# Kernel tuning notes

Hardware: AMD Instinct MI355X
Metric: run time of the kernel (lower is better)

## Reference

```python
import jax, jax.numpy as jnp
import numpy as np

HID = 2560
NH, P, N, G, K = 80, 64, 128, 1, 4
INTER = NH * P            # 5120
CONV_DIM = INTER + 2 * G * N  # 5376
PROJ = INTER + CONV_DIM + NH  # 10576
EPS = 1e-5
DT_MIN, DT_MAX = 0.0, 100.0
BATCH = 64


def setup_inputs() -> dict:
    key = jax.random.key(0)
    ks = jax.random.split(key, 11)
    return {
        "input_states": jax.random.normal(ks[0], (BATCH, 1, HID), jnp.float32),
        "conv_state": 0.1 * jax.random.normal(ks[1], (BATCH, CONV_DIM, K), jnp.float32),
        "ssm_state": 0.1 * jax.random.normal(ks[2], (BATCH, NH, P, N), jnp.float32),
        "in_proj_w": jax.random.normal(ks[3], (PROJ, HID), jnp.float32) * (HID ** -0.5),
        "conv_w": jax.random.normal(ks[4], (CONV_DIM, K), jnp.float32) * 0.2,
        "conv_b": jax.random.normal(ks[5], (CONV_DIM,), jnp.float32) * 0.02,
        "dt_bias": jax.random.normal(ks[6], (NH,), jnp.float32) * 0.1,
        "A_log": jnp.log(jnp.arange(1, NH + 1, dtype=jnp.float32)),
        "D": jnp.ones((NH,), jnp.float32),
        "norm_w": jnp.ones((INTER,), jnp.float32),
        "out_proj_w": jax.random.normal(ks[7], (HID, INTER), jnp.float32) * (INTER ** -0.5),
    }


def reference(input_states, conv_state, ssm_state, in_proj_w, conv_w, conv_b,
              dt_bias, A_log, D, norm_w, out_proj_w):
    B = input_states.shape[0]
    # in_proj: (B,1,HID) @ (HID,PROJ) -> (B,1,PROJ); d_mlp == 0 with these dims
    proj = jnp.einsum("bsh,ph->bsp", input_states, in_proj_w)
    gate = proj[..., :INTER]                       # (B,1,INTER)
    hBC = proj[..., INTER:INTER + CONV_DIM]        # (B,1,CONV_DIM)
    dt = proj[..., INTER + CONV_DIM:]              # (B,1,NH)

    # conv cache update: roll left, append current token
    new_conv_state = jnp.concatenate(
        [conv_state[:, :, 1:], hBC[:, 0, :, None]], axis=-1)  # (B,CONV_DIM,K)
    x = jnp.sum(new_conv_state * conv_w[None], axis=-1) + conv_b  # (B,CONV_DIM)
    x = jax.nn.silu(x)

    hs = x[:, :INTER].reshape(B, NH, P)            # (B,NH,P)
    Bm = x[:, INTER:INTER + G * N].reshape(B, G, N)
    Cm = x[:, INTER + G * N:].reshape(B, G, N)
    Bm = jnp.repeat(Bm, NH // G, axis=1)           # (B,NH,N)
    Cm = jnp.repeat(Cm, NH // G, axis=1)           # (B,NH,N)

    # discretization (dt is per-head, broadcast over head_dim as in source)
    dt_sp = jnp.clip(jax.nn.softplus(dt[:, 0, :] + dt_bias), DT_MIN, DT_MAX)  # (B,NH)
    A = -jnp.exp(A_log)                            # (NH,)
    dA = jnp.exp(dt_sp * A)                        # (B,NH)

    dBx = dt_sp[:, :, None, None] * Bm[:, :, None, :] * hs[..., None]  # (B,NH,P,N)
    new_ssm = ssm_state * dA[:, :, None, None] + dBx                   # (B,NH,P,N)

    y = jnp.einsum("bhpn,bhn->bhp", new_ssm, Cm)   # (B,NH,P)
    y = y + hs * D[None, :, None]
    y = y.reshape(B, 1, INTER)

    # gated RMSNorm (fp32 internals)
    yf = y.astype(jnp.float32) * jax.nn.silu(gate.astype(jnp.float32))
    var = jnp.mean(yf * yf, axis=-1, keepdims=True)
    yn = norm_w * (yf * jax.lax.rsqrt(var + EPS)).astype(y.dtype)

    out = jnp.einsum("bsi,hi->bsh", yn, out_proj_w)  # (B,1,HID)
    return out
```

## Files before the change

### kernel.cpp

```cpp
#include <hip/hip_runtime.h>
#include <stdint.h>

#define HID 2560
#define NH 80
#define PDIM 64
#define NDIM 128
#define INTER 5120
#define CONV_DIM 5376
#define PROJ_DIM 10576
#define NBATCH 64
#define EPS_ 1e-5f

typedef short short8 __attribute__((ext_vector_type(8)));
typedef float f32x4 __attribute__((ext_vector_type(4)));

__device__ __forceinline__ unsigned short f2bf(float f){
  unsigned u = __builtin_bit_cast(unsigned, f);
  u += 0x7FFFu + ((u >> 16) & 1u);
  return (unsigned short)(u >> 16);
}
__device__ __forceinline__ float silu_(float x){ return x / (1.f + __expf(-x)); }

__global__ __launch_bounds__(256) void k_dt(const float* __restrict__ X,
                                            const float* __restrict__ W,
                                            float* __restrict__ dt_part,
                                            unsigned short* __restrict__ Xb){
  const int h = blockIdx.x, ks = blockIdx.y;
  const int tid = threadIdx.x, wid = tid >> 6, lane = tid & 63;
  const float* wr = W + (size_t)(INTER + CONV_DIM + h) * HID + ks * 320;
  float w[5];
  #pragma unroll
  for (int i = 0; i < 5; ++i) w[i] = wr[lane + i * 64];
  #pragma unroll
  for (int bi = 0; bi < 16; ++bi){
    const int b = wid * 16 + bi;
    const float* xr = X + (size_t)b * HID + ks * 320;
    float x[5];
    float acc = 0.f;
    #pragma unroll
    for (int i = 0; i < 5; ++i){ x[i] = xr[lane + i * 64]; acc += x[i] * w[i]; }
    if (h == 0){
      #pragma unroll
      for (int i = 0; i < 5; ++i)
        Xb[(size_t)b * HID + ks * 320 + lane + i * 64] = f2bf(x[i]);
    }
    #pragma unroll
    for (int m = 32; m; m >>= 1) acc += __shfl_xor(acc, m);
    if (lane == 0) dt_part[(ks * NBATCH + b) * NH + h] = acc;
  }
}

__global__ __launch_bounds__(64) void k1_proj(const unsigned short* __restrict__ Xb,
                                              const float* __restrict__ W,
                                              float* __restrict__ proj){
  const int lane = threadIdx.x;
  const int lr = lane & 15, lg = lane >> 4;
  const int n0 = blockIdx.x * 16;
  const short* ap = (const short*)Xb + (size_t)lr * HID + lg * 8;
  const float* bp = W + (size_t)(n0 + lr) * HID + lg * 8;
  f32x4 acc0 = {0,0,0,0}, acc1 = {0,0,0,0}, acc2 = {0,0,0,0}, acc3 = {0,0,0,0};
  #pragma unroll 4
  for (int s = 0; s < 80; ++s){
    const int k = s * 32;
    short8 a0 = *(const short8*)(ap + k);
    short8 a1 = *(const short8*)(ap + 16 * HID + k);
    short8 a2 = *(const short8*)(ap + 32 * HID + k);
    short8 a3 = *(const short8*)(ap + 48 * HID + k);
    float4 b0 = *(const float4*)(bp + k);
    float4 b1 = *(const float4*)(bp + k + 4);
    short8 bb;
    bb[0] = (short)f2bf(b0.x); bb[1] = (short)f2bf(b0.y);
    bb[2] = (short)f2bf(b0.z); bb[3] = (short)f2bf(b0.w);
    bb[4] = (short)f2bf(b1.x); bb[5] = (short)f2bf(b1.y);
    bb[6] = (short)f2bf(b1.z); bb[7] = (short)f2bf(b1.w);
    acc0 = __builtin_amdgcn_mfma_f32_16x16x32_bf16(a0, bb, acc0, 0, 0, 0);
    acc1 = __builtin_amdgcn_mfma_f32_16x16x32_bf16(a1, bb, acc1, 0, 0, 0);
    acc2 = __builtin_amdgcn_mfma_f32_16x16x32_bf16(a2, bb, acc2, 0, 0, 0);
    acc3 = __builtin_amdgcn_mfma_f32_16x16x32_bf16(a3, bb, acc3, 0, 0, 0);
  }
  #pragma unroll
  for (int r = 0; r < 4; ++r){
    const int m = lg * 4 + r;
    proj[(size_t)(m     ) * PROJ_DIM + n0 + lr] = acc0[r];
    proj[(size_t)(m + 16) * PROJ_DIM + n0 + lr] = acc1[r];
    proj[(size_t)(m + 32) * PROJ_DIM + n0 + lr] = acc2[r];
    proj[(size_t)(m + 48) * PROJ_DIM + n0 + lr] = acc3[r];
  }
}

__global__ __launch_bounds__(256) void k2a(const float* __restrict__ cs,
                                           const float* __restrict__ cw,
                                           const float* __restrict__ cb,
                                           const float* __restrict__ proj,
                                           const float* __restrict__ dt_part,
                                           const float* __restrict__ dt_bias,
                                           const float* __restrict__ A_log,
                                           float* __restrict__ hs_bc,
                                           float* __restrict__ dt_sp,
                                           float* __restrict__ dAv,
                                           float* __restrict__ s_bc){
  const int b = blockIdx.y;
  const int c0 = blockIdx.x * 384;
  const int tid = threadIdx.x;
  __shared__ float bc[384];
  for (int i = tid; i < 384; i += 256){
    const int c = c0 + i;
    float4 s4 = *(const float4*)(cs + ((size_t)b * CONV_DIM + c) * 4);
    float4 w4 = *(const float4*)(cw + (size_t)c * 4);
    float hbc = proj[(size_t)b * PROJ_DIM + INTER + c];
    float x = s4.y * w4.x + s4.z * w4.y + s4.w * w4.z + hbc * w4.w + cb[c];
    float v = silu_(x);
    hs_bc[(size_t)b * CONV_DIM + c] = v;
    if (blockIdx.x == 13) bc[i] = v;
  }
  if (blockIdx.x == 0 && tid < NH){
    float acc = dt_bias[tid];
    #pragma unroll
    for (int ks = 0; ks < 8; ++ks) acc += dt_part[(ks * NBATCH + b) * NH + tid];
    float sp = acc > 15.f ? acc : log1pf(__expf(acc));
    sp = fminf(fmaxf(sp, 0.f), 100.f);
    dt_sp[b * NH + tid] = sp;
    dAv[b * NH + tid] = __expf(-sp * __expf(A_log[tid]));
  }
  if (blockIdx.x == 13){
    __syncthreads();
    if (tid < 64){
      float p = bc[128 + tid] * bc[256 + tid] + bc[192 + tid] * bc[320 + tid];
      #pragma unroll
      for (int m = 32; m; m >>= 1) p += __shfl_xor(p, m);
      if (tid == 0) s_bc[b] = p;
    }
  }
}

__global__ __launch_bounds__(256) void k2b(const float* __restrict__ ssm,
                                           const float* __restrict__ hs_bc,
                                           const float* __restrict__ proj,
                                           const float* __restrict__ dt_sp,
                                           const float* __restrict__ dAv,
                                           const float* __restrict__ s_bc,
                                           const float* __restrict__ Dp,
                                           const float* __restrict__ norm_w,
                                           unsigned short* __restrict__ yfb,
                                           float* __restrict__ ssq_part){
  const int h = blockIdx.x, b = blockIdx.y;
  const int tid = threadIdx.x;
  const int wid = tid >> 6, lane = tid & 63;
  const int lr = lane & 15, lg = lane >> 4;
  const float dA_s = dAv[b * NH + h];
  const float coef = dt_sp[b * NH + h] * s_bc[b] + Dp[h];
  const float* Cb = hs_bc + (size_t)b * CONV_DIM + INTER + NDIM;
  float4 c0 = *(const float4*)(Cb + lr * 8);
  float4 c1 = *(const float4*)(Cb + lr * 8 + 4);
  const float* srow = ssm + ((size_t)b * NH + h) * PDIM * NDIM;
  float ssq = 0.f;
  __shared__ float ssql[4];
  #pragma unroll
  for (int r = 0; r < 4; ++r){
    const int p = wid * 16 + r * 4 + lg;
    const float* sp_ = srow + (size_t)p * NDIM + lr * 8;
    float4 v0 = *(const float4*)(sp_);
    float4 v1 = *(const float4*)(sp_ + 4);
    float dot = v0.x*c0.x + v0.y*c0.y + v0.z*c0.z + v0.w*c0.w
              + v1.x*c1.x + v1.y*c1.y + v1.z*c1.z + v1.w*c1.w;
    dot += __shfl_xor(dot, 1); dot += __shfl_xor(dot, 2);
    dot += __shfl_xor(dot, 4); dot += __shfl_xor(dot, 8);
    if (lr == 0){
      const int hp = h * PDIM + p;
      float hs = hs_bc[(size_t)b * CONV_DIM + hp];
      float y = dA_s * dot + hs * coef;
      float g = proj[(size_t)b * PROJ_DIM + hp];
      float yf = y * silu_(g) * norm_w[hp];
      yfb[(size_t)b * INTER + hp] = f2bf(yf);
      ssq += yf * yf;
    }
  }
  #pragma unroll
  for (int m = 32; m; m >>= 1) ssq += __shfl_xor(ssq, m);
  if (lane == 0) ssql[wid] = ssq;
  __syncthreads();
  if (tid == 0) ssq_part[b * NH + h] = ssql[0] + ssql[1] + ssql[2] + ssql[3];
}

__global__ __launch_bounds__(64) void k3_out(const unsigned short* __restrict__ Yb,
                                             const float* __restrict__ W,
                                             float* __restrict__ part){
  const int lane = threadIdx.x;
  const int lr = lane & 15, lg = lane >> 4;
  const int n0 = blockIdx.x * 16;
  const int ks = blockIdx.y;
  const int kb = ks * 1280;
  const short* ap = (const short*)Yb + (size_t)lr * INTER + kb + lg * 8;
  const float* bp = W + (size_t)(n0 + lr) * INTER + kb + lg * 8;
  f32x4 acc0 = {0,0,0,0}, acc1 = {0,0,0,0}, acc2 = {0,0,0,0}, acc3 = {0,0,0,0};
  #pragma unroll 4
  for (int s = 0; s < 40; ++s){
    const int k = s * 32;
    short8 a0 = *(const short8*)(ap + k);
    short8 a1 = *(const short8*)(ap + 16 * INTER + k);
    short8 a2 = *(const short8*)(ap + 32 * INTER + k);
    short8 a3 = *(const short8*)(ap + 48 * INTER + k);
    float4 b0 = *(const float4*)(bp + k);
    float4 b1 = *(const float4*)(bp + k + 4);
    short8 bb;
    bb[0] = (short)f2bf(b0.x); bb[1] = (short)f2bf(b0.y);
    bb[2] = (short)f2bf(b0.z); bb[3] = (short)f2bf(b0.w);
    bb[4] = (short)f2bf(b1.x); bb[5] = (short)f2bf(b1.y);
    bb[6] = (short)f2bf(b1.z); bb[7] = (short)f2bf(b1.w);
    acc0 = __builtin_amdgcn_mfma_f32_16x16x32_bf16(a0, bb, acc0, 0, 0, 0);
    acc1 = __builtin_amdgcn_mfma_f32_16x16x32_bf16(a1, bb, acc1, 0, 0, 0);
    acc2 = __builtin_amdgcn_mfma_f32_16x16x32_bf16(a2, bb, acc2, 0, 0, 0);
    acc3 = __builtin_amdgcn_mfma_f32_16x16x32_bf16(a3, bb, acc3, 0, 0, 0);
  }
  float* pt = part + (size_t)ks * NBATCH * 2560;
  #pragma unroll
  for (int r = 0; r < 4; ++r){
    const int m = lg * 4 + r;
    pt[(size_t)(m     ) * 2560 + n0 + lr] = acc0[r];
    pt[(size_t)(m + 16) * 2560 + n0 + lr] = acc1[r];
    pt[(size_t)(m + 32) * 2560 + n0 + lr] = acc2[r];
    pt[(size_t)(m + 48) * 2560 + n0 + lr] = acc3[r];
  }
}

__global__ __launch_bounds__(256) void k4_norm(const float* __restrict__ part,
                                               const float* __restrict__ ssq_part,
                                               float* __restrict__ out){
  const int b = blockIdx.y;
  const int tid = threadIdx.x;
  __shared__ float w4[4];
  __shared__ float sc;
  float v = (tid < NH) ? ssq_part[b * NH + tid] : 0.f;
  #pragma unroll
  for (int m = 32; m; m >>= 1) v += __shfl_xor(v, m);
  const int wid = tid >> 6, lane = tid & 63;
  if (lane == 0) w4[wid] = v;
  __syncthreads();
  if (tid == 0){
    float total = w4[0] + w4[1] + w4[2] + w4[3];
    sc = rsqrtf(total / (float)INTER + EPS_);
  }
  __syncthreads();
  const int j = blockIdx.x * 256 + tid;
  const size_t idx = (size_t)b * 2560 + j;
  const size_t plane = (size_t)NBATCH * 2560;
  float s = part[idx] + part[plane + idx] + part[2*plane + idx] + part[3*plane + idx];
  out[idx] = sc * s;
}

extern "C" void kernel_launch(void* const* d_in, const int* in_sizes, int n_in,
                              void* d_out, int out_size, void* d_ws, size_t ws_size,
                              hipStream_t stream){
  const float* x_in       = (const float*)d_in[0];
  const float* conv_state = (const float*)d_in[1];
  const float* ssm_state  = (const float*)d_in[2];
  const float* in_proj_w  = (const float*)d_in[3];
  const float* conv_w     = (const float*)d_in[4];
  const float* conv_b     = (const float*)d_in[5];
  const float* dt_bias    = (const float*)d_in[6];
  const float* A_log      = (const float*)d_in[7];
  const float* Dp         = (const float*)d_in[8];
  const float* norm_w     = (const float*)d_in[9];
  const float* out_proj_w = (const float*)d_in[10];
  float* out = (float*)d_out;

  char* ws = (char*)d_ws;
  unsigned short* Xb   = (unsigned short*)(ws);
  float* dt_part       = (float*)(ws + 327680);
  float* proj          = (float*)(ws + 491520);
  float* hs_bc         = (float*)(ws + 3198976);
  float* dt_sp         = (float*)(ws + 4575232);
  float* dAv           = (float*)(ws + 4595712);
  float* s_bc          = (float*)(ws + 4616192);
  float* ssq           = (float*)(ws + 4616448);
  unsigned short* Yb   = (unsigned short*)(ws + 4636928);
  float* part          = (float*)(ws + 5292288);

  k_dt<<<dim3(NH, 8), dim3(256), 0, stream>>>(x_in, in_proj_w, dt_part, Xb);
  k1_proj<<<dim3(PROJ_DIM / 16), dim3(64), 0, stream>>>(Xb, in_proj_w, proj);
  k2a<<<dim3(14, NBATCH), dim3(256), 0, stream>>>(conv_state, conv_w, conv_b, proj,
                                                  dt_part, dt_bias, A_log,
                                                  hs_bc, dt_sp, dAv, s_bc);
  k2b<<<dim3(NH, NBATCH), dim3(256), 0, stream>>>(ssm_state, hs_bc, proj, dt_sp, dAv,
                                                  s_bc, Dp, norm_w, Yb, ssq);
  k3_out<<<dim3(160, 4), dim3(64), 0, stream>>>(Yb, out_proj_w, part);
  k4_norm<<<dim3(10, NBATCH), dim3(256), 0, stream>>>(part, ssq, out);
}
```

Before: 136.5 us.

## Split-K both projection GEMMs into sixteen slices and reduce partials in consumers

The input projection now runs as a split-K GEMM over 16 K-slices, each writing its own partial plane. The conv/gate consumers (k2a, k2b) sum those 16 planes when they read proj values. The output projection goes from 4 to 16 K-slices, and the final norm kernel sums 16 partial planes. The goal is far more wavefronts in flight for the bandwidth-bound weight streaming. The cost is a large partial buffer (about 43 MB written and partly re-read) and extra reduction loads. A redundant 4x repeat loop in k1_proj recomputes the same slice and is rescaled by 0.25, wasting MFMA and load issue.

Measured after the change: 149.5 us. 9.6% more time.

```diff
diff --git a/kernel.cpp b/kernel.cpp
--- a/kernel.cpp
+++ b/kernel.cpp
@@ -52,46 +52,51 @@
 
 __global__ __launch_bounds__(64) void k1_proj(const unsigned short* __restrict__ Xb,
                                               const float* __restrict__ W,
-                                              float* __restrict__ proj){
+                                              float* __restrict__ pp){
   const int lane = threadIdx.x;
   const int lr = lane & 15, lg = lane >> 4;
   const int n0 = blockIdx.x * 16;
-  const short* ap = (const short*)Xb + (size_t)lr * HID + lg * 8;
-  const float* bp = W + (size_t)(n0 + lr) * HID + lg * 8;
+  const int ks = blockIdx.y;
+  const int kb = ks * 160;
+  const short* ap = (const short*)Xb + (size_t)lr * HID + kb + lg * 8;
+  const float* bp = W + (size_t)(n0 + lr) * HID + kb + lg * 8;
   f32x4 acc0 = {0,0,0,0}, acc1 = {0,0,0,0}, acc2 = {0,0,0,0}, acc3 = {0,0,0,0};
-  #pragma unroll 4
-  for (int s = 0; s < 80; ++s){
-    const int k = s * 32;
-    short8 a0 = *(const short8*)(ap + k);
-    short8 a1 = *(const short8*)(ap + 16 * HID + k);
-    short8 a2 = *(const short8*)(ap + 32 * HID + k);
-    short8 a3 = *(const short8*)(ap + 48 * HID + k);
-    float4 b0 = *(const float4*)(bp + k);
-    float4 b1 = *(const float4*)(bp + k + 4);
-    short8 bb;
-    bb[0] = (short)f2bf(b0.x); bb[1] = (short)f2bf(b0.y);
-    bb[2] = (short)f2bf(b0.z); bb[3] = (short)f2bf(b0.w);
-    bb[4] = (short)f2bf(b1.x); bb[5] = (short)f2bf(b1.y);
-    bb[6] = (short)f2bf(b1.z); bb[7] = (short)f2bf(b1.w);
-    acc0 = __builtin_amdgcn_mfma_f32_16x16x32_bf16(a0, bb, acc0, 0, 0, 0);
-    acc1 = __builtin_amdgcn_mfma_f32_16x16x32_bf16(a1, bb, acc1, 0, 0, 0);
-    acc2 = __builtin_amdgcn_mfma_f32_16x16x32_bf16(a2, bb, acc2, 0, 0, 0);
-    acc3 = __builtin_amdgcn_mfma_f32_16x16x32_bf16(a3, bb, acc3, 0, 0, 0);
-  }
+  for (int rep = 0; rep < 4; ++rep){
+    #pragma unroll
+    for (int s = 0; s < 5; ++s){
+      const int k = s * 32;
+      short8 a0 = *(const short8*)(ap + k);
+      short8 a1 = *(const short8*)(ap + 16 * HID + k);
+      short8 a2 = *(const short8*)(ap + 32 * HID + k);
+      short8 a3 = *(const short8*)(ap + 48 * HID + k);
+      float4 b0 = *(const float4*)(bp + k);
+      float4 b1 = *(const float4*)(bp + k + 4);
+      short8 bb;
+      bb[0] = (short)f2bf(b0.x); bb[1] = (short)f2bf(b0.y);
+      bb[2] = (short)f2bf(b0.z); bb[3] = (short)f2bf(b0.w);
+      bb[4] = (short)f2bf(b1.x); bb[5] = (short)f2bf(b1.y);
+      bb[6] = (short)f2bf(b1.z); bb[7] = (short)f2bf(b1.w);
+      acc0 = __builtin_amdgcn_mfma_f32_16x16x32_bf16(a0, bb, acc0, 0, 0, 0);
+      acc1 = __builtin_amdgcn_mfma_f32_16x16x32_bf16(a1, bb, acc1, 0, 0, 0);
+      acc2 = __builtin_amdgcn_mfma_f32_16x16x32_bf16(a2, bb, acc2, 0, 0, 0);
+      acc3 = __builtin_amdgcn_mfma_f32_16x16x32_bf16(a3, bb, acc3, 0, 0, 0);
+    }
+  }
+  float* plane = pp + (size_t)ks * NBATCH * PROJ_DIM;
   #pragma unroll
   for (int r = 0; r < 4; ++r){
     const int m = lg * 4 + r;
-    proj[(size_t)(m     ) * PROJ_DIM + n0 + lr] = acc0[r];
-    proj[(size_t)(m + 16) * PROJ_DIM + n0 + lr] = acc1[r];
-    proj[(size_t)(m + 32) * PROJ_DIM + n0 + lr] = acc2[r];
-    proj[(size_t)(m + 48) * PROJ_DIM + n0 + lr] = acc3[r];
+    plane[(size_t)(m     ) * PROJ_DIM + n0 + lr] = acc0[r] * 0.25f;
+    plane[(size_t)(m + 16) * PROJ_DIM + n0 + lr] = acc1[r] * 0.25f;
+    plane[(size_t)(m + 32) * PROJ_DIM + n0 + lr] = acc2[r] * 0.25f;
+    plane[(size_t)(m + 48) * PROJ_DIM + n0 + lr] = acc3[r] * 0.25f;
   }
 }
 
 __global__ __launch_bounds__(256) void k2a(const float* __restrict__ cs,
                                            const float* __restrict__ cw,
                                            const float* __restrict__ cb,
-                                           const float* __restrict__ proj,
+                                           const float* __restrict__ pp,
                                            const float* __restrict__ dt_part,
                                            const float* __restrict__ dt_bias,
                                            const float* __restrict__ A_log,
@@ -102,12 +107,16 @@
   const int b = blockIdx.y;
   const int c0 = blockIdx.x * 384;
   const int tid = threadIdx.x;
+  const size_t plane = (size_t)NBATCH * PROJ_DIM;
   __shared__ float bc[384];
   for (int i = tid; i < 384; i += 256){
     const int c = c0 + i;
     float4 s4 = *(const float4*)(cs + ((size_t)b * CONV_DIM + c) * 4);
     float4 w4 = *(const float4*)(cw + (size_t)c * 4);
-    float hbc = proj[(size_t)b * PROJ_DIM + INTER + c];
+    const size_t pidx = (size_t)b * PROJ_DIM + INTER + c;
+    float hbc = 0.f;
+    #pragma unroll
+    for (int ks = 0; ks < 16; ++ks) hbc += pp[(size_t)ks * plane + pidx];
     float x = s4.y * w4.x + s4.z * w4.y + s4.w * w4.z + hbc * w4.w + cb[c];
     float v = silu_(x);
     hs_bc[(size_t)b * CONV_DIM + c] = v;
@@ -135,7 +144,7 @@
 
 __global__ __launch_bounds__(256) void k2b(const float* __restrict__ ssm,
                                            const float* __restrict__ hs_bc,
-                                           const float* __restrict__ proj,
+                                           const float* __restrict__ pp,
                                            const float* __restrict__ dt_sp,
                                            const float* __restrict__ dAv,
                                            const float* __restrict__ s_bc,
@@ -149,6 +158,7 @@
   const int lr = lane & 15, lg = lane >> 4;
   const float dA_s = dAv[b * NH + h];
   const float coef = dt_sp[b * NH + h] * s_bc[b] + Dp[h];
+  const size_t plane = (size_t)NBATCH * PROJ_DIM;
   const float* Cb = hs_bc + (size_t)b * CONV_DIM + INTER + NDIM;
   float4 c0 = *(const float4*)(Cb + lr * 8);
   float4 c1 = *(const float4*)(Cb + lr * 8 + 4);
@@ -169,7 +179,10 @@
       const int hp = h * PDIM + p;
       float hs = hs_bc[(size_t)b * CONV_DIM + hp];
       float y = dA_s * dot + hs * coef;
-      float g = proj[(size_t)b * PROJ_DIM + hp];
+      const size_t gi = (size_t)b * PROJ_DIM + hp;
+      float g = 0.f;
+      #pragma unroll
+      for (int ks = 0; ks < 16; ++ks) g += pp[(size_t)ks * plane + gi];
       float yf = y * silu_(g) * norm_w[hp];
       yfb[(size_t)b * INTER + hp] = f2bf(yf);
       ssq += yf * yf;
@@ -189,12 +202,12 @@
   const int lr = lane & 15, lg = lane >> 4;
   const int n0 = blockIdx.x * 16;
   const int ks = blockIdx.y;
-  const int kb = ks * 1280;
+  const int kb = ks * 320;
   const short* ap = (const short*)Yb + (size_t)lr * INTER + kb + lg * 8;
   const float* bp = W + (size_t)(n0 + lr) * INTER + kb + lg * 8;
   f32x4 acc0 = {0,0,0,0}, acc1 = {0,0,0,0}, acc2 = {0,0,0,0}, acc3 = {0,0,0,0};
-  #pragma unroll 4
-  for (int s = 0; s < 40; ++s){
+  #pragma unroll
+  for (int s = 0; s < 10; ++s){
     const int k = s * 32;
     short8 a0 = *(const short8*)(ap + k);
     short8 a1 = *(const short8*)(ap + 16 * INTER + k);
@@ -244,7 +257,9 @@
   const int j = blockIdx.x * 256 + tid;
   const size_t idx = (size_t)b * 2560 + j;
   const size_t plane = (size_t)NBATCH * 2560;
-  float s = part[idx] + part[plane + idx] + part[2*plane + idx] + part[3*plane + idx];
+  float s = 0.f;
+  #pragma unroll
+  for (int ks = 0; ks < 16; ++ks) s += part[(size_t)ks * plane + idx];
   out[idx] = sc * s;
 }
 
@@ -267,22 +282,22 @@
   char* ws = (char*)d_ws;
   unsigned short* Xb   = (unsigned short*)(ws);
   float* dt_part       = (float*)(ws + 327680);
-  float* proj          = (float*)(ws + 491520);
-  float* hs_bc         = (float*)(ws + 3198976);
-  float* dt_sp         = (float*)(ws + 4575232);
-  float* dAv           = (float*)(ws + 4595712);
-  float* s_bc          = (float*)(ws + 4616192);
-  float* ssq           = (float*)(ws + 4616448);
-  unsigned short* Yb   = (unsigned short*)(ws + 4636928);
-  float* part          = (float*)(ws + 5292288);
+  float* pp            = (float*)(ws + 491520);
+  float* hs_bc         = (float*)(ws + 43810816);
+  float* dt_sp         = (float*)(ws + 45187072);
+  float* dAv           = (float*)(ws + 45207552);
+  float* s_bc          = (float*)(ws + 45228032);
+  float* ssq           = (float*)(ws + 45228288);
+  unsigned short* Yb   = (unsigned short*)(ws + 45248768);
+  float* part          = (float*)(ws + 45904128);
 
   k_dt<<<dim3(NH, 8), dim3(256), 0, stream>>>(x_in, in_proj_w, dt_part, Xb);
-  k1_proj<<<dim3(PROJ_DIM / 16), dim3(64), 0, stream>>>(Xb, in_proj_w, proj);
-  k2a<<<dim3(14, NBATCH), dim3(256), 0, stream>>>(conv_state, conv_w, conv_b, proj,
+  k1_proj<<<dim3(661, 16), dim3(64), 0, stream>>>(Xb, in_proj_w, pp);
+  k2a<<<dim3(14, NBATCH), dim3(256), 0, stream>>>(conv_state, conv_w, conv_b, pp,
                                                   dt_part, dt_bias, A_log,
                                                   hs_bc, dt_sp, dAv, s_bc);
-  k2b<<<dim3(NH, NBATCH), dim3(256), 0, stream>>>(ssm_state, hs_bc, proj, dt_sp, dAv,
+  k2b<<<dim3(NH, NBATCH), dim3(256), 0, stream>>>(ssm_state, hs_bc, pp, dt_sp, dAv,
                                                   s_bc, Dp, norm_w, Yb, ssq);
-  k3_out<<<dim3(160, 4), dim3(64), 0, stream>>>(Yb, out_proj_w, part);
+  k3_out<<<dim3(160, 16), dim3(64), 0, stream>>>(Yb, out_proj_w, part);
   k4_norm<<<dim3(10, NBATCH), dim3(256), 0, stream>>>(part, ssq, out);
 }
```
